# Kernel optimization log

Hardware: AMD Instinct MI355X
Metric: run time of the kernel (lower is better)

Reference implementation:

```python
import jax, jax.numpy as jnp
import numpy as np

D_MODEL = 4096
EXPERTS = 64
TOPK = 2


def setup_inputs() -> dict:
    key = jax.random.key(0)
    kx, kw = jax.random.split(key)
    x = jax.random.normal(kx, (4, 4096, D_MODEL), dtype=jnp.float32)
    # nn.Linear(input_size, expert_num, bias=False) weight, stored as [D, E] for x @ W
    W = jax.random.normal(kw, (D_MODEL, EXPERTS), dtype=jnp.float32) * (1.0 / np.sqrt(D_MODEL))
    return {"x": x, "W": W}


def reference(x, W):
    # logits = GateL(x): [B, S, E]
    logits = jnp.einsum("bsd,de->bse", x, W)
    y = jax.nn.softmax(logits, axis=-1)
    # top-k mask: scatter ones at top-k expert slots, zero elsewhere
    _, topk_idx = jax.lax.top_k(y, TOPK)            # [B, S, k]
    mask = jnp.sum(jax.nn.one_hot(topk_idx, EXPERTS, dtype=y.dtype), axis=-2)  # [B, S, E]
    y = y * mask
    return (y, logits)
```

## Files before the change

### kernel.cpp

```cpp
#include <hip/hip_runtime.h>
#include <hip/hip_bf16.h>


typedef float f32x4 __attribute__((ext_vector_type(4)));
typedef __bf16 bf16x8 __attribute__((ext_vector_type(8)));

#define MFMA16(a, b, c) __builtin_amdgcn_mfma_f32_16x16x32_bf16((a), (b), (c), 0, 0, 0)

__global__ __launch_bounds__(256) void k_prep_w(const float* __restrict__ W,
                                                __bf16* __restrict__ wsW) {
  const int kc = blockIdx.x;
  const int t = threadIdx.x;
  const int kk0 = t >> 4;
  const int n0 = (t & 15) << 2;
  for (int i = 0; i < 2; ++i) {
    const int kk = kk0 + (i << 4);
    const float4 w4 = *(const float4*)(W + (size_t)(kc * 32 + kk) * 64 + n0);
    const float f[4] = {w4.x, w4.y, w4.z, w4.w};
    for (int j = 0; j < 4; ++j) {
      const int n = n0 + j;
      const __bf16 h = (__bf16)f[j];
      const __bf16 l = (__bf16)(f[j] - (float)h);
      const int base = (kc << 12) + ((n >> 4) << 9) + ((n & 15) << 5) + kk;
      wsW[base] = h;
      wsW[base + 2048] = l;
    }
  }
}

__global__ __launch_bounds__(256, 2) void k_gate(const float* __restrict__ x,
                                                 const __bf16* __restrict__ wsW,
                                                 float* __restrict__ y,
                                                 float* __restrict__ logits) {
  const int t = threadIdx.x;
  const int w = t >> 6, l = t & 63;
  const int tb = blockIdx.x * 32;
  const int mt = w & 1, nh = w >> 1;
  const int q = l >> 4, ln = l & 15;

  const float* xp = x + (size_t)(tb + mt * 16 + ln) * 4096 + q * 8;
  const __bf16* wp = wsW + (nh * 2) * 512 + ln * 32 + q * 8;

  f32x4 acc0 = {0.f, 0.f, 0.f, 0.f};
  f32x4 acc1 = {0.f, 0.f, 0.f, 0.f};

  float4 xa0, xb0, xa1, xb1;
  bf16x8 h0_0, l0_0, h1_0, l1_0;
  bf16x8 h0_1, l0_1, h1_1, l1_1;

#define LOAD_STAGE(S, c) do {                                          \
    xa##S = *(const float4*)(xp + (size_t)(c) * 32);                   \
    xb##S = *(const float4*)(xp + (size_t)(c) * 32 + 4);               \
    h0_##S = *(const bf16x8*)(wp + (size_t)(c) * 4096);                \
    l0_##S = *(const bf16x8*)(wp + (size_t)(c) * 4096 + 2048);         \
    h1_##S = *(const bf16x8*)(wp + (size_t)(c) * 4096 + 512);          \
    l1_##S = *(const bf16x8*)(wp + (size_t)(c) * 4096 + 2560);         \
  } while (0)

#define COMPUTE(S) do {                                                \
    bf16x8 ah, al;                                                     \
    const float f[8] = {xa##S.x, xa##S.y, xa##S.z, xa##S.w,            \
                        xb##S.x, xb##S.y, xb##S.z, xb##S.w};           \
    _Pragma("unroll")                                                  \
    for (int i = 0; i < 8; ++i) {                                      \
      const __bf16 hh = (__bf16)f[i];                                  \
      ah[i] = hh;                                                      \
      al[i] = (__bf16)(f[i] - (float)hh);                              \
    }                                                                  \
    acc0 = MFMA16(ah, h0_##S, acc0);                                   \
    acc0 = MFMA16(al, h0_##S, acc0);                                   \
    acc0 = MFMA16(ah, l0_##S, acc0);                                   \
    acc1 = MFMA16(ah, h1_##S, acc1);                                   \
    acc1 = MFMA16(al, h1_##S, acc1);                                   \
    acc1 = MFMA16(ah, l1_##S, acc1);                                   \
  } while (0)

  LOAD_STAGE(0, 0);
  LOAD_STAGE(1, 1);
  for (int c = 0; c < 128; c += 2) {
    COMPUTE(0);
    if (c + 2 < 128) LOAD_STAGE(0, c + 2);
    COMPUTE(1);
    if (c + 3 < 128) LOAD_STAGE(1, c + 3);
  }
#undef LOAD_STAGE
#undef COMPUTE

  __shared__ float lt[32 * 65];
  const int col = nh * 32 + ln;
#pragma unroll
  for (int r = 0; r < 4; ++r) {
    const int row = mt * 16 + q * 4 + r;
    lt[row * 65 + col] = acc0[r];
    lt[row * 65 + col + 16] = acc1[r];
    logits[(size_t)(tb + row) * 64 + col] = acc0[r];
    logits[(size_t)(tb + row) * 64 + col + 16] = acc1[r];
  }
  __syncthreads();

#pragma unroll
  for (int i = 0; i < 8; ++i) {
    const int tok = w * 8 + i;
    const float v = lt[tok * 65 + l];
    float bv = v; int bi = l;
    for (int off = 32; off; off >>= 1) {
      const float ov = __shfl_xor(bv, off);
      const int oi = __shfl_xor(bi, off);
      if (ov > bv || (ov == bv && oi < bi)) { bv = ov; bi = oi; }
    }
    const int i1 = bi;
    const float m1 = bv;
    float cv = (l == i1) ? -3.402823466e38f : v;
    int ci = l;
    for (int off = 32; off; off >>= 1) {
      const float ov = __shfl_xor(cv, off);
      const int oi = __shfl_xor(ci, off);
      if (ov > cv || (ov == cv && oi < ci)) { cv = ov; ci = oi; }
    }
    const float e = __expf(v - m1);
    float s = e;
    for (int off = 32; off; off >>= 1) s += __shfl_xor(s, off);
    y[(size_t)(tb + tok) * 64 + l] = (l == i1 || l == ci) ? (e / s) : 0.0f;
  }
}

extern "C" void kernel_launch(void* const* d_in, const int* in_sizes, int n_in,
                              void* d_out, int out_size, void* d_ws, size_t ws_size,
                              hipStream_t stream) {
  (void)in_sizes; (void)n_in; (void)out_size; (void)ws_size;
  const float* x = (const float*)d_in[0];
  const float* W = (const float*)d_in[1];
  float* out = (float*)d_out;
  float* yout = out;
  float* logits = out + 1048576;
  __bf16* wsW = (__bf16*)d_ws;

  k_prep_w<<<128, 256, 0, stream>>>(W, wsW);
  k_gate<<<512, 256, 0, stream>>>(x, wsW, yout, logits);
}
```

Before: 409.9 us.

## Deepen gate GEMM pipeline to four stages and add lo*lo MFMA term

Rearranges the bf16 hi/lo weight workspace so each lane's four weight fragments sit contiguously. The main loop becomes a four-stage software pipeline with pointer increments instead of two stages with conditional loads. The hi/lo split of x now uses bit truncation rather than round-to-nearest conversion. A fourth lo*lo MFMA per accumulator is added, which costs more matrix work per chunk in return for closer fp32 accuracy. The deeper prefetch is meant to hide global load latency in this memory-bound kernel, at the cost of more registers held live.

```diff
diff --git a/kernel.cpp b/kernel.cpp
--- a/kernel.cpp
+++ b/kernel.cpp
@@ -21,10 +21,21 @@
       const int n = n0 + j;
       const __bf16 h = (__bf16)f[j];
       const __bf16 l = (__bf16)(f[j] - (float)h);
-      const int base = (kc << 12) + ((n >> 4) << 9) + ((n & 15) << 5) + kk;
+      const int base = (kc << 12) + ((n >> 4) << 10) + ((n & 15) << 5) + kk;
       wsW[base] = h;
-      wsW[base + 2048] = l;
+      wsW[base + 512] = l;
     }
+  }
+}
+
+__device__ __forceinline__ void split8(const float4 a, const float4 b,
+                                       bf16x8& hi, bf16x8& lo) {
+  const float f[8] = {a.x, a.y, a.z, a.w, b.x, b.y, b.z, b.w};
+#pragma unroll
+  for (int i = 0; i < 8; ++i) {
+    const unsigned u = __builtin_bit_cast(unsigned, f[i]);
+    hi[i] = __builtin_bit_cast(__bf16, (unsigned short)(u >> 16));
+    lo[i] = (__bf16)(f[i] - __builtin_bit_cast(float, u & 0xFFFF0000u));
   }
 }
 
@@ -39,52 +50,56 @@
   const int q = l >> 4, ln = l & 15;
 
   const float* xp = x + (size_t)(tb + mt * 16 + ln) * 4096 + q * 8;
-  const __bf16* wp = wsW + (nh * 2) * 512 + ln * 32 + q * 8;
+  const __bf16* wq = wsW + nh * 2048 + ln * 32 + q * 8;
+  const __bf16* wp0 = wq;
+  const __bf16* wp1 = wq + 4096;
+  const __bf16* wp2 = wq + 8192;
+  const __bf16* wp3 = wq + 12288;
 
   f32x4 acc0 = {0.f, 0.f, 0.f, 0.f};
   f32x4 acc1 = {0.f, 0.f, 0.f, 0.f};
 
-  float4 xa0, xb0, xa1, xb1;
-  bf16x8 h0_0, l0_0, h1_0, l1_0;
-  bf16x8 h0_1, l0_1, h1_1, l1_1;
+  float4 xa[4], xb[4];
+  bf16x8 wh0[4], wl0[4], wh1[4], wl1[4];
 
-#define LOAD_STAGE(S, c) do {                                          \
-    xa##S = *(const float4*)(xp + (size_t)(c) * 32);                   \
-    xb##S = *(const float4*)(xp + (size_t)(c) * 32 + 4);               \
-    h0_##S = *(const bf16x8*)(wp + (size_t)(c) * 4096);                \
-    l0_##S = *(const bf16x8*)(wp + (size_t)(c) * 4096 + 2048);         \
-    h1_##S = *(const bf16x8*)(wp + (size_t)(c) * 4096 + 512);          \
-    l1_##S = *(const bf16x8*)(wp + (size_t)(c) * 4096 + 2560);         \
+#define LOADX(S) do {                                                   \
+    xa[S] = *(const float4*)(xp + (S) * 32);                            \
+    xb[S] = *(const float4*)(xp + (S) * 32 + 4);                        \
+  } while (0)
+#define LOADW(S, P) do {                                                \
+    wh0[S] = *(const bf16x8*)((P));                                     \
+    wl0[S] = *(const bf16x8*)((P) + 512);                               \
+    wh1[S] = *(const bf16x8*)((P) + 1024);                              \
+    wl1[S] = *(const bf16x8*)((P) + 1536);                              \
+  } while (0)
+#define COMP(S) do {                                                    \
+    bf16x8 ah, al;                                                      \
+    split8(xa[S], xb[S], ah, al);                                       \
+    acc0 = MFMA16(ah, wh0[S], acc0);                                    \
+    acc0 = MFMA16(al, wh0[S], acc0);                                    \
+    acc0 = MFMA16(ah, wl0[S], acc0);                                    \
+    acc0 = MFMA16(al, wl0[S], acc0);                                    \
+    acc1 = MFMA16(ah, wh1[S], acc1);                                    \
+    acc1 = MFMA16(al, wh1[S], acc1);                                    \
+    acc1 = MFMA16(ah, wl1[S], acc1);                                    \
+    acc1 = MFMA16(al, wl1[S], acc1);                                    \
   } while (0)
 
-#define COMPUTE(S) do {                                                \
-    bf16x8 ah, al;                                                     \
-    const float f[8] = {xa##S.x, xa##S.y, xa##S.z, xa##S.w,            \
-                        xb##S.x, xb##S.y, xb##S.z, xb##S.w};           \
-    _Pragma("unroll")                                                  \
-    for (int i = 0; i < 8; ++i) {                                      \
-      const __bf16 hh = (__bf16)f[i];                                  \
-      ah[i] = hh;                                                      \
-      al[i] = (__bf16)(f[i] - (float)hh);                              \
-    }                                                                  \
-    acc0 = MFMA16(ah, h0_##S, acc0);                                   \
-    acc0 = MFMA16(al, h0_##S, acc0);                                   \
-    acc0 = MFMA16(ah, l0_##S, acc0);                                   \
-    acc1 = MFMA16(ah, h1_##S, acc1);                                   \
-    acc1 = MFMA16(al, h1_##S, acc1);                                   \
-    acc1 = MFMA16(ah, l1_##S, acc1);                                   \
-  } while (0)
+  LOADX(0); LOADX(1); LOADX(2); LOADX(3);
+  LOADW(0, wp0); LOADW(1, wp1); LOADW(2, wp2); LOADW(3, wp3);
+  xp += 128; wp0 += 16384; wp1 += 16384; wp2 += 16384; wp3 += 16384;
 
-  LOAD_STAGE(0, 0);
-  LOAD_STAGE(1, 1);
-  for (int c = 0; c < 128; c += 2) {
-    COMPUTE(0);
-    if (c + 2 < 128) LOAD_STAGE(0, c + 2);
-    COMPUTE(1);
-    if (c + 3 < 128) LOAD_STAGE(1, c + 3);
+  for (int it = 0; it < 31; ++it) {
+    COMP(0); LOADX(0); LOADW(0, wp0);
+    COMP(1); LOADX(1); LOADW(1, wp1);
+    COMP(2); LOADX(2); LOADW(2, wp2);
+    COMP(3); LOADX(3); LOADW(3, wp3);
+    xp += 128; wp0 += 16384; wp1 += 16384; wp2 += 16384; wp3 += 16384;
   }
-#undef LOAD_STAGE
-#undef COMPUTE
+  COMP(0); COMP(1); COMP(2); COMP(3);
+#undef LOADX
+#undef LOADW
+#undef COMP
 
   __shared__ float lt[32 * 65];
   const int col = nh * 32 + ln;
```

Result: no change. 404.5 us (-1.3%).
